# Kernel optimization log

Hardware: AMD Instinct MI355X
Metric: run time of the kernel (lower is better)

## Reference

```python
import jax, jax.numpy as jnp
import numpy as np
import math

D_MODEL = 2048
N_HEADS = 16
D_HEAD = D_MODEL // N_HEADS
MAX_T = 2048
B, T = 2, 2048


def rotate_half(x):
    # interleaved rotate: (x0,x1,x2,x3,...) -> (-x1,x0,-x3,x2,...)
    x1 = x[..., ::2]
    x2 = x[..., 1::2]
    return jnp.stack((-x2, x1), axis=-1).reshape(x.shape)


def setup_inputs() -> dict:
    key = jax.random.key(0)
    k1, k2, k3 = jax.random.split(key, 3)
    x = jax.random.normal(k1, (B, T, D_MODEL), dtype=jnp.float32)
    # torch nn.Linear weights: [out, in]
    s = 1.0 / math.sqrt(D_MODEL)
    Wqkv = jax.random.uniform(k2, (3 * D_MODEL, D_MODEL), dtype=jnp.float32, minval=-s, maxval=s)
    WO = jax.random.uniform(k3, (D_MODEL, D_MODEL), dtype=jnp.float32, minval=-s, maxval=s)
    return {"x": x, "Wqkv": Wqkv, "WO": WO}


def reference(x, Wqkv, WO):
    Bx, Tx, _ = x.shape
    # RoPE tables (buffers)
    pos = jnp.arange(Tx, dtype=jnp.float32)
    freqs = jnp.exp(-math.log(10000.0) * jnp.arange(0, D_HEAD, 2, dtype=jnp.float32) / D_HEAD)
    angles = pos[:, None] * freqs[None, :]               # [T, d_head/2]
    sin = jnp.repeat(jnp.sin(angles), 2, axis=-1)        # [T, d_head]
    cos = jnp.repeat(jnp.cos(angles), 2, axis=-1)
    sin = sin[None, None, :, :]
    cos = cos[None, None, :, :]

    qkv = x @ Wqkv.T                                     # [B, T, 3D]
    q, k, v = jnp.split(qkv, 3, axis=-1)
    def to_heads(t):
        return t.reshape(Bx, Tx, N_HEADS, D_HEAD).transpose(0, 2, 1, 3)  # [B,H,T,d]
    q, k, v = to_heads(q), to_heads(k), to_heads(v)

    q = q * cos + rotate_half(q) * sin
    k = k * cos + rotate_half(k) * sin

    scores = jnp.einsum('bhqd,bhkd->bhqk', q, k) / math.sqrt(D_HEAD)
    mask = jnp.triu(jnp.full((Tx, Tx), -jnp.inf, dtype=scores.dtype), k=1)
    scores = scores + mask
    attn = jax.nn.softmax(scores, axis=-1)
    out = jnp.einsum('bhqk,bhkd->bhqd', attn, v)
    out = out.transpose(0, 2, 1, 3).reshape(Bx, Tx, D_MODEL)
    return out @ WO.T
```

## Files before the change

kernel.cpp:

```cpp
#include <hip/hip_runtime.h>
#include <hip/hip_bf16.h>

typedef unsigned short u16;
typedef __attribute__((ext_vector_type(8))) short bf16x8;
typedef __attribute__((ext_vector_type(4))) float f32x4;

#define B_   2
#define T_   2048
#define DM   2048
#define NH   16
#define DH   128
#define NQKV 6144

__device__ __forceinline__ u16 f2bf(float f) {
  __hip_bfloat16 h = __float2bfloat16(f);
  u16 u; __builtin_memcpy(&u, &h, 2); return u;
}
__device__ __forceinline__ float bf2f(u16 u) {
  __hip_bfloat16 h; __builtin_memcpy(&h, &u, 2); return __bfloat162float(h);
}
__device__ __forceinline__ void gl_lds16(const void* g, void* l) {
  __builtin_amdgcn_global_load_lds(
      (__attribute__((address_space(1))) unsigned int*)g,
      (__attribute__((address_space(3))) unsigned int*)l, 16, 0, 0);
}
__device__ __forceinline__ f32x4 MFMA(bf16x8 a, bf16x8 b, f32x4 c) {
  return __builtin_amdgcn_mfma_f32_16x16x32_bf16(a, b, c, 0, 0, 0);
}

__global__ __launch_bounds__(256) void cast_kernel(const float* __restrict__ in,
                                                   u16* __restrict__ out, int n4) {
  int i = blockIdx.x * 256 + threadIdx.x;
  if (i >= n4) return;
  float4 v = ((const float4*)in)[i];
  ushort4 o;
  o.x = f2bf(v.x); o.y = f2bf(v.y); o.z = f2bf(v.z); o.w = f2bf(v.w);
  ((ushort4*)out)[i] = o;
}

#define G1_M 4096
#define G1_N 6144
#define G1_K 2048

#define MFMA_Q(AQ, M0)                                                        \
  _Pragma("unroll") for (int e_ = 0; e_ < 2; ++e_)                            \
  _Pragma("unroll") for (int n_ = 0; n_ < 4; ++n_)                            \
  _Pragma("unroll") for (int kb_ = 0; kb_ < 2; ++kb_)                         \
    acc[(M0) + e_][n_] = MFMA(AQ[e_][kb_], bfr[n_][kb_], acc[(M0) + e_][n_])

#define BARRIER() asm volatile("s_barrier" ::: "memory")
#define LGKM0()                                                               \
  do {                                                                        \
    asm volatile("s_waitcnt lgkmcnt(0)" ::: "memory");                        \
    __builtin_amdgcn_sched_barrier(0);                                        \
  } while (0)

__global__ __launch_bounds__(512, 2) void gemm1_8ph(const u16* __restrict__ A,
                                                    const u16* __restrict__ Bm,
                                                    u16* __restrict__ C) {
  __shared__ alignas(16) u16 As[2][256 * 64];
  __shared__ alignas(16) u16 Bs[2][256 * 64];
  const int tid = threadIdx.x;
  const int w = tid >> 6, lane = tid & 63;
  const int lrow = lane & 15, quad = lane >> 4;
  const long tileM = (long)blockIdx.y * 256, tileN = (long)blockIdx.x * 256;
  const int wm = (w >> 2) * 128, wn = (w & 3) * 64;

  const int sw8 = w * 8;
  const int srowL = lane >> 3;
  const int schunk = ((lane & 7) ^ srowL) * 8;
  const u16* Ag0 = A + (tileM + sw8 + srowL) * (long)G1_K + schunk;
  const u16* Bg0 = Bm + (tileN + sw8 + srowL) * (long)G1_K + schunk;

  auto stgA = [&](int tt, int h) {
    const int b = tt & 1;
    gl_lds16(Ag0 + (size_t)(h * 128) * G1_K + tt * 64,
             &As[b][(h * 128 + sw8) * 64]);
    gl_lds16(Ag0 + (size_t)(h * 128 + 64) * G1_K + tt * 64,
             &As[b][(h * 128 + 64 + sw8) * 64]);
  };
  auto stgB = [&](int tt, int h) {
    const int b = tt & 1;
    gl_lds16(Bg0 + (size_t)(h * 128) * G1_K + tt * 64,
             &Bs[b][(h * 128 + sw8) * 64]);
    gl_lds16(Bg0 + (size_t)(h * 128 + 64) * G1_K + tt * 64,
             &Bs[b][(h * 128 + 64 + sw8) * 64]);
  };

  const int aBase = (wm + lrow) * 64;
  const int bBase = (wn + lrow) * 64;
  const int slot[2] = { (quad ^ (lrow & 7)) * 8, ((4 + quad) ^ (lrow & 7)) * 8 };

  f32x4 acc[8][4] = {};

  stgA(0, 0); stgA(0, 1); stgB(0, 0); stgB(0, 1);
  stgB(1, 0); stgB(1, 1); stgA(1, 0);
  asm volatile("s_waitcnt vmcnt(6)" ::: "memory");
  BARRIER();

#pragma unroll 1
  for (int t = 0; t < 32; ++t) {
    const u16* AsC = As[t & 1];
    const u16* BsC = Bs[t & 1];
    bf16x8 aF[2][2], bfr[4][2];
#pragma unroll
    for (int ni = 0; ni < 4; ++ni)
#pragma unroll
      for (int kb = 0; kb < 2; ++kb)
        bfr[ni][kb] = *(const bf16x8*)(BsC + bBase + ni * 1024 + slot[kb]);
#pragma unroll
    for (int e = 0; e < 2; ++e)
#pragma unroll
      for (int kb = 0; kb < 2; ++kb)
        aF[e][kb] = *(const bf16x8*)(AsC + aBase + e * 1024 + slot[kb]);
    BARRIER();
    LGKM0();
    __builtin_amdgcn_s_setprio(1);
    MFMA_Q(aF, 0);
    __builtin_amdgcn_s_setprio(0);
    if (t + 1 < 32) stgA(t + 1, 1);
    BARRIER();
#pragma unroll
    for (int e = 0; e < 2; ++e)
#pragma unroll
      for (int kb = 0; kb < 2; ++kb)
        aF[e][kb] = *(const bf16x8*)(AsC + aBase + (2 + e) * 1024 + slot[kb]);
    BARRIER();
    LGKM0();
    __builtin_amdgcn_s_setprio(1);
    MFMA_Q(aF, 2);
    __builtin_amdgcn_s_setprio(0);
    if (t + 2 < 32) stgB(t + 2, 0);
    BARRIER();
#pragma unroll
    for (int e = 0; e < 2; ++e)
#pragma unroll
      for (int kb = 0; kb < 2; ++kb)
        aF[e][kb] = *(const bf16x8*)(AsC + aBase + (4 + e) * 1024 + slot[kb]);
    BARRIER();
    LGKM0();
    __builtin_amdgcn_s_setprio(1);
    MFMA_Q(aF, 4);
    __builtin_amdgcn_s_setprio(0);
    if (t + 2 < 32) stgB(t + 2, 1);
    BARRIER();
#pragma unroll
    for (int e = 0; e < 2; ++e)
#pragma unroll
      for (int kb = 0; kb < 2; ++kb)
        aF[e][kb] = *(const bf16x8*)(AsC + aBase + (6 + e) * 1024 + slot[kb]);
    BARRIER();
    LGKM0();
    __builtin_amdgcn_s_setprio(1);
    MFMA_Q(aF, 6);
    __builtin_amdgcn_s_setprio(0);
    if (t + 2 < 32) stgA(t + 2, 0);
    if (t < 30) { asm volatile("s_waitcnt vmcnt(6)" ::: "memory"); }
    else if (t == 30) { asm volatile("s_waitcnt vmcnt(0)" ::: "memory"); }
    BARRIER();
  }

  const long crow = tileM + wm + quad * 4;
  const long ccol = tileN + wn + lrow;
#pragma unroll
  for (int mi = 0; mi < 8; ++mi)
#pragma unroll
    for (int ni = 0; ni < 4; ++ni)
#pragma unroll
      for (int r = 0; r < 4; ++r)
        C[(crow + mi * 16 + r) * (long)G1_N + (ccol + ni * 16)] =
            f2bf(acc[mi][ni][r]);
}

__global__ __launch_bounds__(256) void gemm_bt(const u16* __restrict__ A,
                                               const u16* __restrict__ Bm,
                                               void* __restrict__ Cp,
                                               int M, int N, int K, int out_f32) {
  __shared__ u16 As[128 * 64];
  __shared__ u16 Bs[128 * 64];
  const int tid  = threadIdx.x;
  const int wave = tid >> 6, lane = tid & 63;
  const int lrow = lane & 15, quad = lane >> 4;
  const long tileM = (long)blockIdx.y * 128, tileN = (long)blockIdx.x * 128;
  const int wm = (wave >> 1) * 64, wn = (wave & 1) * 64;
  const int sRowIn = lane >> 3;
  const int sChunk = (lane & 7) ^ sRowIn;
  const int sRow0  = wave * 32 + sRowIn;
  const u16* Ag = A + (tileM + sRow0) * (long)K + sChunk * 8;
  const u16* Bg = Bm + (tileN + sRow0) * (long)K + sChunk * 8;
  u16* AsW = As + wave * 2048;
  u16* BsW = Bs + wave * 2048;
  f32x4 acc[4][4] = {};
  for (int kt = 0; kt < K; kt += 64) {
#pragma unroll
    for (int i = 0; i < 4; ++i)
      gl_lds16(Ag + kt + (size_t)i * 8 * K, AsW + i * 512);
#pragma unroll
    for (int i = 0; i < 4; ++i)
      gl_lds16(Bg + kt + (size_t)i * 8 * K, BsW + i * 512);
    __syncthreads();
#pragma unroll
    for (int kb = 0; kb < 2; ++kb) {
      const int slot8 = (((kb * 4 + quad) ^ (lrow & 7)) * 8);
      bf16x8 af[4], bfr[4];
#pragma unroll
      for (int i = 0; i < 4; ++i)
        af[i]  = *(const bf16x8*)(As + (wm + i * 16 + lrow) * 64 + slot8);
#pragma unroll
      for (int i = 0; i < 4; ++i)
        bfr[i] = *(const bf16x8*)(Bs + (wn + i * 16 + lrow) * 64 + slot8);
#pragma unroll
      for (int mi = 0; mi < 4; ++mi)
#pragma unroll
        for (int ni = 0; ni < 4; ++ni)
          acc[mi][ni] = MFMA(af[mi], bfr[ni], acc[mi][ni]);
    }
    __syncthreads();
  }
  const long crow = tileM + wm + quad * 4;
  const long ccol = tileN + wn + lrow;
  if (out_f32) {
    float* C = (float*)Cp;
#pragma unroll
    for (int mi = 0; mi < 4; ++mi)
#pragma unroll
      for (int ni = 0; ni < 4; ++ni)
#pragma unroll
        for (int r = 0; r < 4; ++r)
          C[(crow + mi * 16 + r) * (long)N + (ccol + ni * 16)] = acc[mi][ni][r];
  } else {
    u16* C = (u16*)Cp;
#pragma unroll
    for (int mi = 0; mi < 4; ++mi)
#pragma unroll
      for (int ni = 0; ni < 4; ++ni)
#pragma unroll
        for (int r = 0; r < 4; ++r)
          C[(crow + mi * 16 + r) * (long)N + (ccol + ni * 16)] = f2bf(acc[mi][ni][r]);
  }
}

__global__ __launch_bounds__(256) void rope_reorder(const u16* __restrict__ qkv,
                                                    u16* __restrict__ Q,
                                                    u16* __restrict__ Kd,
                                                    u16* __restrict__ Vt) {
  const int tt = blockIdx.x;
  const int bh = blockIdx.y;
  const int b = bh >> 4, h = bh & 15;
  const int tid = threadIdx.x;
  __shared__ u16 vlds[64 * 129];
  const float qscale = 0.08838834764831845f;
#pragma unroll
  for (int it = 0; it < 16; ++it) {
    int p  = tid + it * 256;
    int tl = p >> 6;
    int i  = p & 63;
    int t  = tt * 64 + tl;
    float freq  = __expf(-9.210340371976184f * (float)i / 64.0f);
    float angle = (float)t * freq;
    float sn, cs;
    sincosf(angle, &sn, &cs);
    const u16* row = qkv + (size_t)(b * T_ + t) * NQKV;
    size_t qo = ((size_t)bh * T_ + t) * DH + 2 * i;
    float q0 = bf2f(row[h * DH + 2 * i]), q1 = bf2f(row[h * DH + 2 * i + 1]);
    Q[qo]     = f2bf((q0 * cs - q1 * sn) * qscale);
    Q[qo + 1] = f2bf((q1 * cs + q0 * sn) * qscale);
    float k0 = bf2f(row[DM + h * DH + 2 * i]), k1 = bf2f(row[DM + h * DH + 2 * i + 1]);
    Kd[qo]     = f2bf(k0 * cs - k1 * sn);
    Kd[qo + 1] = f2bf(k1 * cs + k0 * sn);
  }
#pragma unroll
  for (int it = 0; it < 32; ++it) {
    int idx = tid + it * 256;
    int tl = idx >> 7, d = idx & 127;
    vlds[tl * 129 + d] =
        qkv[(size_t)(b * T_ + tt * 64 + tl) * NQKV + 2 * DM + h * DH + d];
  }
  __syncthreads();
#pragma unroll
  for (int it = 0; it < 32; ++it) {
    int idx = tid + it * 256;
    int d = idx >> 6, tl = idx & 63;
    Vt[((size_t)bh * DH + d) * T_ + tt * 64 + tl] = vlds[tl * 129 + d];
  }
}

__global__ __launch_bounds__(256) void attn_flash(const u16* __restrict__ Q,
                                                  const u16* __restrict__ K,
                                                  const u16* __restrict__ Vt,
                                                  u16* __restrict__ AO) {
  __shared__ u16 Kl[64 * 128];
  __shared__ u16 Vl[128 * 64];
  __shared__ u16 Pl[4 * 16 * 64];
  const int pairIdx = blockIdx.x;
  const int bh = blockIdx.y;
  const int b = bh >> 4, h = bh & 15;
  const int tid = threadIdx.x;
  const int wave = tid >> 6, lane = tid & 63;
  const int lrow = lane & 15, quad = lane >> 4;
  const u16* Qb = Q + (size_t)bh * T_ * DH;
  const u16* Kb = K + (size_t)bh * T_ * DH;
  const u16* Vb = Vt + (size_t)bh * DH * T_;

  u16* KlW = Kl + wave * 2048;
  u16* VlW = Vl + wave * 2048;
  const int kRowIn = lane >> 4;
  const int vRowIn = lane >> 3;
  const int vChunk = (lane & 7) ^ vRowIn;
  u16* PlW = Pl + wave * 1024;

  for (int pass = 0; pass < 2; ++pass) {
    const int qt = pass == 0 ? (2 * gridDim.x - 1 - pairIdx) : pairIdx;
    const int qbase = qt * 64;

    bf16x8 qf[4];
    {
      const u16* qrow = Qb + (size_t)(qbase + wave * 16 + lrow) * DH + quad * 8;
#pragma unroll
      for (int kc = 0; kc < 4; ++kc) qf[kc] = *(const bf16x8*)(qrow + kc * 32);
    }
    f32x4 o[8] = {};
    float lsum[4] = {0.f, 0.f, 0.f, 0.f};

    for (int j = 0; j <= qt; ++j) {
#pragma unroll
      for (int i = 0; i < 4; ++i) {
        int krow = wave * 16 + i * 4 + kRowIn;
        int kch = (lane & 15) ^ (i * 4 + kRowIn);
        gl_lds16(Kb + (size_t)(j * 64 + krow) * DH + kch * 8, KlW + i * 512);
      }
#pragma unroll
      for (int i = 0; i < 4; ++i) {
        int vd = wave * 32 + i * 8 + vRowIn;
        gl_lds16(Vb + (size_t)vd * T_ + j * 64 + vChunk * 8, VlW + i * 512);
      }
      __syncthreads();

      f32x4 s[4] = {};
#pragma unroll
      for (int kc = 0; kc < 4; ++kc)
#pragma unroll
        for (int ns = 0; ns < 4; ++ns) {
          bf16x8 kf = *(const bf16x8*)(Kl + (ns * 16 + lrow) * 128 +
                                       (((kc * 4 + quad) ^ lrow) * 8));
          s[ns] = MFMA(qf[kc], kf, s[ns]);
        }
      if (j == qt) {
#pragma unroll
        for (int ns = 0; ns < 4; ++ns)
#pragma unroll
          for (int r = 0; r < 4; ++r)
            if (ns * 16 + lrow > wave * 16 + quad * 4 + r) s[ns][r] = -__builtin_inff();
      }
#pragma unroll
      for (int r = 0; r < 4; ++r) {
        const int prow = quad * 4 + r;
#pragma unroll
        for (int ns = 0; ns < 4; ++ns) {
          float p = __expf(s[ns][r]);
          PlW[prow * 64 + (((ns * 2 + (lrow >> 3)) ^ (prow & 7)) * 8) +
              (lrow & 7)] = f2bf(p);
          lsum[r] += p;
        }
      }

#pragma unroll
      for (int kc = 0; kc < 2; ++kc) {
        bf16x8 pf = *(const bf16x8*)(PlW + lrow * 64 +
                                     (((kc * 4 + quad) ^ (lrow & 7)) * 8));
#pragma unroll
        for (int os = 0; os < 8; ++os) {
          bf16x8 vf = *(const bf16x8*)(Vl + (os * 16 + lrow) * 64 +
                                       (((kc * 4 + quad) ^ (lrow & 7)) * 8));
          o[os] = MFMA(pf, vf, o[os]);
        }
      }
      __syncthreads();
    }
#pragma unroll
    for (int r = 0; r < 4; ++r) {
      lsum[r] += __shfl_xor(lsum[r], 1, 16);
      lsum[r] += __shfl_xor(lsum[r], 2, 16);
      lsum[r] += __shfl_xor(lsum[r], 4, 16);
      lsum[r] += __shfl_xor(lsum[r], 8, 16);
    }
#pragma unroll
    for (int r = 0; r < 4; ++r) {
      float inv = 1.0f / lsum[r];
      const size_t row = (size_t)b * T_ + qbase + wave * 16 + quad * 4 + r;
      u16* dst = AO + row * DM + h * DH;
#pragma unroll
      for (int os = 0; os < 8; ++os) dst[os * 16 + lrow] = f2bf(o[os][r] * inv);
    }
  }
}

extern "C" void kernel_launch(void* const* d_in, const int* in_sizes, int n_in,
                              void* d_out, int out_size, void* d_ws, size_t ws_size,
                              hipStream_t stream) {
  const float* x    = (const float*)d_in[0];
  const float* Wqkv = (const float*)d_in[1];
  const float* WO   = (const float*)d_in[2];
  char* ws = (char*)d_ws;
  size_t off = 0;
  u16* xb   = (u16*)(ws + off); off += (size_t)B_ * T_ * DM * 2;
  u16* wqb  = (u16*)(ws + off); off += (size_t)NQKV * DM * 2;
  u16* wob  = (u16*)(ws + off); off += (size_t)DM * DM * 2;
  u16* qkvb = (u16*)(ws + off); off += (size_t)B_ * T_ * NQKV * 2;
  u16* Qb   = (u16*)(ws + off); off += (size_t)B_ * NH * T_ * DH * 2;
  u16* Kb   = (u16*)(ws + off); off += (size_t)B_ * NH * T_ * DH * 2;
  u16* Vtb  = (u16*)(ws + off); off += (size_t)B_ * NH * T_ * DH * 2;
  u16* AO   = xb;

  cast_kernel<<<(B_ * T_ * DM / 4 + 255) / 256, 256, 0, stream>>>(x, xb, B_ * T_ * DM / 4);
  cast_kernel<<<(NQKV * DM / 4 + 255) / 256, 256, 0, stream>>>(Wqkv, wqb, NQKV * DM / 4);
  cast_kernel<<<(DM * DM / 4 + 255) / 256, 256, 0, stream>>>(WO, wob, DM * DM / 4);

  gemm1_8ph<<<dim3(G1_N / 256, G1_M / 256), 512, 0, stream>>>(xb, wqb, qkvb);

  rope_reorder<<<dim3(T_ / 64, B_ * NH), 256, 0, stream>>>(qkvb, Qb, Kb, Vtb);

  attn_flash<<<dim3(T_ / 128, B_ * NH), 256, 0, stream>>>(Qb, Kb, Vtb, AO);

  gemm_bt<<<dim3(DM / 128, B_ * T_ / 128), 256, 0, stream>>>(
      AO, wob, d_out, B_ * T_, DM, DM, 1);
}
```

Before: 414.6 us.

## Double-buffer A fragments in registers and halve barriers in QKV GEMM main loop

Restructures the 8-phase QKV projection GEMM loop so the LDS reads for the next quarter of A fragments (and the next tile's B/A fragments) are issued right after the current MFMA block, using two register fragment sets. This cuts the number of s_barrier calls per iteration from eight to four and overlaps LDS reads with MFMA work. The global-load wait counts are moved and changed (vmcnt 4 placed before the last phase), which alters the prefetch ordering and raises register pressure under the 2-blocks-per-CU launch bound. Any mistake in the new wait placement could create LDS read/write races.

```diff
diff --git a/kernel.cpp b/kernel.cpp
--- a/kernel.cpp
+++ b/kernel.cpp
@@ -54,6 +54,7 @@
     asm volatile("s_waitcnt lgkmcnt(0)" ::: "memory");                        \
     __builtin_amdgcn_sched_barrier(0);                                        \
   } while (0)
+#define SBAR() __builtin_amdgcn_sched_barrier(0)
 
 __global__ __launch_bounds__(512, 2) void gemm1_8ph(const u16* __restrict__ A,
                                                     const u16* __restrict__ Bm,
@@ -92,71 +93,85 @@
   const int slot[2] = { (quad ^ (lrow & 7)) * 8, ((4 + quad) ^ (lrow & 7)) * 8 };
 
   f32x4 acc[8][4] = {};
+  bf16x8 bfr[4][2];
+  bf16x8 aCur[2][2], aNxt[2][2];
 
   stgA(0, 0); stgA(0, 1); stgB(0, 0); stgB(0, 1);
   stgB(1, 0); stgB(1, 1); stgA(1, 0);
   asm volatile("s_waitcnt vmcnt(6)" ::: "memory");
   BARRIER();
+#pragma unroll
+  for (int ni = 0; ni < 4; ++ni)
+#pragma unroll
+    for (int kb = 0; kb < 2; ++kb)
+      bfr[ni][kb] = *(const bf16x8*)(Bs[0] + bBase + ni * 1024 + slot[kb]);
+#pragma unroll
+  for (int e = 0; e < 2; ++e)
+#pragma unroll
+    for (int kb = 0; kb < 2; ++kb)
+      aCur[e][kb] = *(const bf16x8*)(As[0] + aBase + e * 1024 + slot[kb]);
 
 #pragma unroll 1
   for (int t = 0; t < 32; ++t) {
     const u16* AsC = As[t & 1];
-    const u16* BsC = Bs[t & 1];
-    bf16x8 aF[2][2], bfr[4][2];
-#pragma unroll
-    for (int ni = 0; ni < 4; ++ni)
+    LGKM0();
+    __builtin_amdgcn_s_setprio(1);
+    MFMA_Q(aCur, 0);
+    __builtin_amdgcn_s_setprio(0);
+    SBAR();
+#pragma unroll
+    for (int e = 0; e < 2; ++e)
 #pragma unroll
       for (int kb = 0; kb < 2; ++kb)
-        bfr[ni][kb] = *(const bf16x8*)(BsC + bBase + ni * 1024 + slot[kb]);
-#pragma unroll
-    for (int e = 0; e < 2; ++e)
-#pragma unroll
-      for (int kb = 0; kb < 2; ++kb)
-        aF[e][kb] = *(const bf16x8*)(AsC + aBase + e * 1024 + slot[kb]);
+        aNxt[e][kb] = *(const bf16x8*)(AsC + aBase + (2 + e) * 1024 + slot[kb]);
+    if (t + 1 < 32) stgA(t + 1, 1);
     BARRIER();
     LGKM0();
     __builtin_amdgcn_s_setprio(1);
-    MFMA_Q(aF, 0);
+    MFMA_Q(aNxt, 2);
     __builtin_amdgcn_s_setprio(0);
-    if (t + 1 < 32) stgA(t + 1, 1);
-    BARRIER();
+    SBAR();
 #pragma unroll
     for (int e = 0; e < 2; ++e)
 #pragma unroll
       for (int kb = 0; kb < 2; ++kb)
-        aF[e][kb] = *(const bf16x8*)(AsC + aBase + (2 + e) * 1024 + slot[kb]);
+        aCur[e][kb] = *(const bf16x8*)(AsC + aBase + (4 + e) * 1024 + slot[kb]);
+    if (t + 2 < 32) stgB(t + 2, 0);
     BARRIER();
     LGKM0();
     __builtin_amdgcn_s_setprio(1);
-    MFMA_Q(aF, 2);
+    MFMA_Q(aCur, 4);
     __builtin_amdgcn_s_setprio(0);
-    if (t + 2 < 32) stgB(t + 2, 0);
-    BARRIER();
+    SBAR();
 #pragma unroll
     for (int e = 0; e < 2; ++e)
 #pragma unroll
       for (int kb = 0; kb < 2; ++kb)
-        aF[e][kb] = *(const bf16x8*)(AsC + aBase + (4 + e) * 1024 + slot[kb]);
+        aNxt[e][kb] = *(const bf16x8*)(AsC + aBase + (6 + e) * 1024 + slot[kb]);
+    if (t + 2 < 32) stgB(t + 2, 1);
+    if (t < 30) { asm volatile("s_waitcnt vmcnt(4)" ::: "memory"); }
+    else       { asm volatile("s_waitcnt vmcnt(0)" ::: "memory"); }
     BARRIER();
     LGKM0();
     __builtin_amdgcn_s_setprio(1);
-    MFMA_Q(aF, 4);
+    MFMA_Q(aNxt, 6);
     __builtin_amdgcn_s_setprio(0);
-    if (t + 2 < 32) stgB(t + 2, 1);
-    BARRIER();
-#pragma unroll
-    for (int e = 0; e < 2; ++e)
-#pragma unroll
-      for (int kb = 0; kb < 2; ++kb)
-        aF[e][kb] = *(const bf16x8*)(AsC + aBase + (6 + e) * 1024 + slot[kb]);
-    BARRIER();
-    LGKM0();
-    __builtin_amdgcn_s_setprio(1);
-    MFMA_Q(aF, 6);
-    __builtin_amdgcn_s_setprio(0);
+    SBAR();
+    if (t + 1 < 32) {
+      const u16* AsN = As[(t + 1) & 1];
+      const u16* BsN = Bs[(t + 1) & 1];
+#pragma unroll
+      for (int ni = 0; ni < 4; ++ni)
+#pragma unroll
+        for (int kb = 0; kb < 2; ++kb)
+          bfr[ni][kb] = *(const bf16x8*)(BsN + bBase + ni * 1024 + slot[kb]);
+#pragma unroll
+      for (int e = 0; e < 2; ++e)
+#pragma unroll
+        for (int kb = 0; kb < 2; ++kb)
+          aCur[e][kb] = *(const bf16x8*)(AsN + aBase + e * 1024 + slot[kb]);
+    }
     if (t + 2 < 32) stgA(t + 2, 0);
-    if (t < 30) { asm volatile("s_waitcnt vmcnt(6)" ::: "memory"); }
-    else if (t == 30) { asm volatile("s_waitcnt vmcnt(0)" ::: "memory"); }
     BARRIER();
   }
 
```

After: 382.9 us. -7.6%, faster.
